# Performance work log

Measured on AMD Instinct MI355X. Metric: run time of the kernel, lower is better.

## Reference

```python
import jax, jax.numpy as jnp
import numpy as np

B, T, D, H = 64, 512, 256, 1024
INIT_S = 0.005


def setup_inputs() -> dict:
    key = jax.random.key(0)
    ks = jax.random.split(key, 8)
    gate_bias = float(np.log(INIT_S / (1.0 - INIT_S)))
    # Linear weights in torch layout [out, in]; y = x @ W.T + b.
    # Gate weights (Ws, Us) are zero-init in the module; we use small random
    # values so the gate path actually exercises the math.
    return {
        "x": jax.random.normal(ks[0], (B, T, D), dtype=jnp.float32),
        "Wx_w": jax.random.normal(ks[1], (H, D), dtype=jnp.float32) / np.sqrt(D),
        "Wx_b": jnp.zeros((H,), dtype=jnp.float32),
        "Wh_w": jax.random.normal(ks[2], (H, H), dtype=jnp.float32) / np.sqrt(H),
        "Ws_w": jax.random.normal(ks[3], (1, D), dtype=jnp.float32) * 0.01,
        "Ws_b": jnp.full((1,), gate_bias, dtype=jnp.float32),
        "Us_w": jax.random.normal(ks[4], (1, H), dtype=jnp.float32) * 0.01,
        "out_w": jax.random.normal(ks[5], (1, H), dtype=jnp.float32) / np.sqrt(H),
        "out_b": jnp.zeros((1,), dtype=jnp.float32),
    }


def reference(x, Wx_w, Wx_b, Wh_w, Ws_w, Ws_b, Us_w, out_w, out_b):
    # SharedGateRNN.forward_with_intermediates (ln=False, gate_rescale=None)
    wh_diag = jnp.diagonal(Wh_w)        # [H]
    us_vec = Us_w.reshape(-1)           # [H]

    def step(h_prev, x_t):
        # x_t: [B, D], h_prev: [B, H]
        a_s = x_t @ Ws_w.T + Ws_b + h_prev @ Us_w.T     # [B, 1]
        s = jax.nn.sigmoid(a_s)                          # [B, 1] scalar gate
        pre = x_t @ Wx_w.T + Wx_b + h_prev @ Wh_w.T      # [B, H]
        h_tilde = jnp.tanh(pre)
        h = (1.0 - s) * h_prev + s * h_tilde             # broadcast gate over H
        y = h @ out_w.T + out_b                          # [B, 1]
        gate_s = jnp.broadcast_to(s, h.shape)
        leak = 1.0 - gate_s
        tanh_prime = 1.0 - h_tilde ** 2
        s_prime = s * (1.0 - s)                          # [B, 1]
        rdiag = (h_tilde - h_prev) * (s_prime * us_vec) + s * tanh_prime * wh_diag
        return h, (y, h, gate_s, leak, rdiag)

    h0 = jnp.zeros((x.shape[0], H), dtype=x.dtype)
    x_t_first = jnp.transpose(x, (1, 0, 2))              # [T, B, D]
    _, (ys, hs, gates, leaks, rdiags) = jax.lax.scan(step, h0, x_t_first)

    swap = lambda a: jnp.transpose(a, (1, 0, 2))         # [T,B,*] -> [B,T,*]
    return (swap(ys), swap(hs), swap(gates), swap(leaks), swap(rdiags))
```

## Files before the change

### kernel.cpp

```cpp
#include <hip/hip_runtime.h>

#define NT 512
#define ND 256
#define NH 1024
#define NB 64

typedef float f32x4 __attribute__((ext_vector_type(4)));
typedef short bf16x8 __attribute__((ext_vector_type(8)));

__device__ __forceinline__ unsigned short f2bf(float f) {
  unsigned u = __builtin_bit_cast(unsigned, f);
  u += 0x7fffu + ((u >> 16) & 1u);
  return (unsigned short)(u >> 16);
}
__device__ __forceinline__ float bflo(unsigned u) {
  return __builtin_bit_cast(float, u << 16);
}
__device__ __forceinline__ float bfhi(unsigned u) {
  return __builtin_bit_cast(float, u & 0xffff0000u);
}
__device__ __forceinline__ bf16x8 pack8(float4 a, float4 b) {
  bf16x8 r;
  r[0] = (short)f2bf(a.x); r[1] = (short)f2bf(a.y);
  r[2] = (short)f2bf(a.z); r[3] = (short)f2bf(a.w);
  r[4] = (short)f2bf(b.x); r[5] = (short)f2bf(b.y);
  r[6] = (short)f2bf(b.z); r[7] = (short)f2bf(b.w);
  return r;
}

__global__ void __launch_bounds__(256, 1)
rnn_step_kernel(const float* __restrict__ x,
                const float* __restrict__ Wx_w,
                const float* __restrict__ Wx_b,
                const float* __restrict__ Wh_w,
                const float* __restrict__ Ws_w,
                const float* __restrict__ Ws_b,
                const float* __restrict__ Us_w,
                float* __restrict__ out,
                unsigned short* __restrict__ hbuf,
                unsigned int* __restrict__ flags)
{
  const int tid = (int)threadIdx.x;
  const int w   = tid >> 6;
  const int l   = tid & 63;
  const int bm  = l & 15;
  const int lg  = l >> 4;
  const int sl  = (int)blockIdx.x & 63;
  const int bg  = (int)blockIdx.x >> 6;
  const int r_base = sl * 16;
  const int b_base = bg * 16;
  const int ro = tid & 15;
  const int bo = tid >> 4;
  const int rg = r_base + ro;
  const int b_glob = b_base + bo;

  __shared__ unsigned short us_sh[1024];
  __shared__ float cpart[4][4][72];
  __shared__ float gpart[4][16];

  {
    const float4 uv = *(const float4*)(Us_w + tid*4);
    us_sh[tid*4+0] = f2bf(uv.x); us_sh[tid*4+1] = f2bf(uv.y);
    us_sh[tid*4+2] = f2bf(uv.z); us_sh[tid*4+3] = f2bf(uv.w);
  }

  bf16x8 whf[8];
  bf16x8 wxf[2];
  float4 wsf[4];
  {
    const int ar = r_base + bm;
    #pragma unroll
    for (int m = 0; m < 8; ++m) {
      const int k0 = w*256 + m*32 + lg*8;
      const float4 f0 = *(const float4*)(Wh_w + (size_t)ar*NH + k0);
      const float4 f1 = *(const float4*)(Wh_w + (size_t)ar*NH + k0 + 4);
      whf[m] = pack8(f0, f1);
    }
    #pragma unroll
    for (int m = 0; m < 2; ++m) {
      const int k0 = w*64 + m*32 + lg*8;
      const float4 f0 = *(const float4*)(Wx_w + (size_t)ar*ND + k0);
      const float4 f1 = *(const float4*)(Wx_w + (size_t)ar*ND + k0 + 4);
      wxf[m] = pack8(f0, f1);
      wsf[m*2]   = *(const float4*)(Ws_w + k0);
      wsf[m*2+1] = *(const float4*)(Ws_w + k0 + 4);
    }
  }
  const float wxb_r = Wx_b[rg];
  const float whd_r = Wh_w[(size_t)rg*NH + rg];
  const float usr_r = Us_w[rg];
  const float wsb   = Ws_b[0];

  float* const hs_o = out + (size_t)NB*NT;
  float* const g_o  = hs_o + (size_t)NB*NT*NH;
  float* const l_o  = g_o  + (size_t)NB*NT*NH;
  float* const rd_o = l_o  + (size_t)NB*NT*NH;

  __syncthreads();

  float myh = 0.f;
  float p_sg = 0.f, p_htld = 0.f, p_hp = 0.f;

  for (int t = 0; t < NT; ++t) {
    f32x4 acc = {0.f, 0.f, 0.f, 0.f};
    float ga = 0.f;
    {
      const float* xrow = x + ((size_t)(b_base+bm)*NT + t)*ND + w*64 + lg*8;
      #pragma unroll
      for (int m = 0; m < 2; ++m) {
        const float4 f0 = *(const float4*)(xrow + m*32);
        const float4 f1 = *(const float4*)(xrow + m*32 + 4);
        acc = __builtin_amdgcn_mfma_f32_16x16x32_bf16(
                wxf[m], pack8(f0, f1), acc, 0, 0, 0);
        ga += wsf[m*2].x*f0.x + wsf[m*2].y*f0.y + wsf[m*2].z*f0.z + wsf[m*2].w*f0.w
            + wsf[m*2+1].x*f1.x + wsf[m*2+1].y*f1.y + wsf[m*2+1].z*f1.z + wsf[m*2+1].w*f1.w;
      }
    }

    if (t > 0) {
      {
        const unsigned int* fp = flags + ((size_t)bg*NT + (t-1))*64 + l;
        while (true) {
          unsigned int v;
          asm volatile("global_load_dword %0, %1, off sc0 sc1\n\t"
                       "s_waitcnt vmcnt(0)"
                       : "=v"(v) : "v"(fp) : "memory");
          if (__all((int)(v != 0u))) break;
          __builtin_amdgcn_s_sleep(1);
        }
      }
      __builtin_amdgcn_sched_barrier(0);
      const unsigned short* hrow =
          hbuf + ((size_t)((t-1)&1)*NB + b_base + bm)*NH + w*256 + lg*8;
      uint4 hv[8];
      #pragma unroll
      for (int m = 0; m < 8; ++m)
        asm volatile("global_load_dwordx4 %0, %1, off sc0 sc1"
                     : "=v"(hv[m]) : "v"(hrow + m*32) : "memory");
      {
        const size_t obase = ((size_t)b_glob*NT + (t-1))*NH + rg;
        const float sp  = p_sg * (1.f - p_sg);
        const float rdv = (p_htld - p_hp)*(sp*usr_r) +
                          p_sg*(1.f - p_htld*p_htld)*whd_r;
        const float lv  = 1.f - p_sg;
        asm volatile("global_store_dword %0, %1, off nt"
                     :: "v"(hs_o + obase), "v"(myh) : "memory");
        asm volatile("global_store_dword %0, %1, off nt"
                     :: "v"(g_o + obase), "v"(p_sg) : "memory");
        asm volatile("global_store_dword %0, %1, off nt"
                     :: "v"(l_o + obase), "v"(lv) : "memory");
        asm volatile("global_store_dword %0, %1, off nt"
                     :: "v"(rd_o + obase), "v"(rdv) : "memory");
      }
      asm volatile("s_waitcnt vmcnt(4)" ::: "memory");
      __builtin_amdgcn_sched_barrier(0);
      #pragma unroll
      for (int m = 0; m < 8; ++m) {
        acc = __builtin_amdgcn_mfma_f32_16x16x32_bf16(
                whf[m], __builtin_bit_cast(bf16x8, hv[m]), acc, 0, 0, 0);
        const uint4 uu = *(const uint4*)&us_sh[w*256 + m*32 + lg*8];
        ga += bflo(uu.x)*bflo(hv[m].x) + bfhi(uu.x)*bfhi(hv[m].x)
            + bflo(uu.y)*bflo(hv[m].y) + bfhi(uu.y)*bfhi(hv[m].y)
            + bflo(uu.z)*bflo(hv[m].z) + bfhi(uu.z)*bfhi(hv[m].z)
            + bflo(uu.w)*bflo(hv[m].w) + bfhi(uu.w)*bfhi(hv[m].w);
      }
    }

    ga += __shfl_xor(ga, 16, 64);
    ga += __shfl_xor(ga, 32, 64);
    if (l < 16) gpart[w][l] = ga;
    cpart[w][0][l] = acc[0];
    cpart[w][1][l] = acc[1];
    cpart[w][2][l] = acc[2];
    cpart[w][3][l] = acc[3];
    __syncthreads();

    const float gsum = gpart[0][bo] + gpart[1][bo] + gpart[2][bo] + gpart[3][bo];
    const int ci = ro & 3, cl = ((ro >> 2) << 4) + bo;
    const float pre0 = cpart[0][ci][cl] + cpart[1][ci][cl] +
                       cpart[2][ci][cl] + cpart[3][ci][cl];
    const float sg   = 1.f / (1.f + expf(-(gsum + wsb)));
    const float pre  = pre0 + wxb_r;
    const float htld = tanhf(pre);
    const float hp   = myh;
    const float h    = (1.f - sg)*hp + sg*htld;
    myh = h; p_sg = sg; p_htld = htld; p_hp = hp;
    {
      const unsigned hb = (unsigned)f2bf(h);
      unsigned short* hptr = hbuf + ((size_t)(t & 1)*NB + b_glob)*NH + rg;
      asm volatile("global_store_short %0, %1, off sc0 sc1"
                   :: "v"(hptr), "v"(hb) : "memory");
    }
    asm volatile("s_waitcnt vmcnt(0)" ::: "memory");
    __syncthreads();
    if (tid == 0) {
      unsigned int one = 1u;
      unsigned int* fp = flags + ((size_t)bg*NT + t)*64 + sl;
      asm volatile("global_store_dword %0, %1, off sc0 sc1"
                   :: "v"(fp), "v"(one) : "memory");
    }
  }

  {
    const size_t obase = ((size_t)b_glob*NT + (NT-1))*NH + rg;
    const float sp  = p_sg * (1.f - p_sg);
    const float rdv = (p_htld - p_hp)*(sp*usr_r) +
                      p_sg*(1.f - p_htld*p_htld)*whd_r;
    __builtin_nontemporal_store(myh, &hs_o[obase]);
    __builtin_nontemporal_store(p_sg, &g_o[obase]);
    __builtin_nontemporal_store(1.f - p_sg, &l_o[obase]);
    __builtin_nontemporal_store(rdv, &rd_o[obase]);
  }
}

__global__ void yfinish_kernel(const float* __restrict__ hs,
                               const float* __restrict__ out_w,
                               const float* __restrict__ out_b,
                               float* __restrict__ ys)
{
  const int row  = (int)blockIdx.x*4 + ((int)threadIdx.x >> 6);
  const int lane = (int)threadIdx.x & 63;
  const float4* hp = (const float4*)(hs + (size_t)row*NH);
  const float4* wp = (const float4*)out_w;
  float s = 0.f;
  #pragma unroll
  for (int i = 0; i < 4; ++i) {
    const float4 h4 = hp[i*64 + lane];
    const float4 w4 = wp[i*64 + lane];
    s += h4.x*w4.x + h4.y*w4.y + h4.z*w4.z + h4.w*w4.w;
  }
  #pragma unroll
  for (int off = 32; off > 0; off >>= 1) s += __shfl_xor(s, off, 64);
  if (lane == 0) ys[row] = s + out_b[0];
}

extern "C" void kernel_launch(void* const* d_in, const int* in_sizes, int n_in,
                              void* d_out, int out_size, void* d_ws, size_t ws_size,
                              hipStream_t stream)
{
  (void)in_sizes; (void)n_in; (void)out_size; (void)ws_size;
  const float* x     = (const float*)d_in[0];
  const float* Wx_w  = (const float*)d_in[1];
  const float* Wx_b  = (const float*)d_in[2];
  const float* Wh_w  = (const float*)d_in[3];
  const float* Ws_w  = (const float*)d_in[4];
  const float* Ws_b  = (const float*)d_in[5];
  const float* Us_w  = (const float*)d_in[6];
  const float* out_w = (const float*)d_in[7];
  const float* out_b = (const float*)d_in[8];
  float* out = (float*)d_out;

  char* ws = (char*)d_ws;
  unsigned short* hbuf = (unsigned short*)ws;
  unsigned int* flags  = (unsigned int*)(ws + 262144);

  hipMemsetAsync(flags, 0, (size_t)4*NT*64*sizeof(unsigned int), stream);
  rnn_step_kernel<<<dim3(256), dim3(256), 0, stream>>>(
      x, Wx_w, Wx_b, Wh_w, Ws_w, Ws_b, Us_w, out, hbuf, flags);
  yfinish_kernel<<<dim3((NB*NT)/4), dim3(256), 0, stream>>>(
      out + (size_t)NB*NT, out_w, out_b, out);
}
```

Measured before the change: 1.819 ms.

## Repartition RNN step across 128 blocks of 512 threads with 32 rows each

```diff
diff --git a/kernel.cpp b/kernel.cpp
--- a/kernel.cpp
+++ b/kernel.cpp
@@ -28,7 +28,7 @@
   return r;
 }
 
-__global__ void __launch_bounds__(256, 1)
+__global__ void __launch_bounds__(512, 1)
 rnn_step_kernel(const float* __restrict__ x,
                 const float* __restrict__ Wx_w,
                 const float* __restrict__ Wx_b,
@@ -45,46 +45,47 @@
   const int l   = tid & 63;
   const int bm  = l & 15;
   const int lg  = l >> 4;
-  const int sl  = (int)blockIdx.x & 63;
-  const int bg  = (int)blockIdx.x >> 6;
-  const int r_base = sl * 16;
+  const int sl  = (int)blockIdx.x & 31;
+  const int bg  = (int)blockIdx.x >> 5;
+  const int r_base = sl * 32;
   const int b_base = bg * 16;
-  const int ro = tid & 15;
-  const int bo = tid >> 4;
+  const int ro = tid & 31;
+  const int bo = tid >> 5;
   const int rg = r_base + ro;
   const int b_glob = b_base + bo;
 
   __shared__ unsigned short us_sh[1024];
-  __shared__ float cpart[4][4][72];
-  __shared__ float gpart[4][16];
-
-  {
+  __shared__ float cpart[8][8][72];
+  __shared__ float gpart[8][16];
+
+  if (tid < 256) {
     const float4 uv = *(const float4*)(Us_w + tid*4);
     us_sh[tid*4+0] = f2bf(uv.x); us_sh[tid*4+1] = f2bf(uv.y);
     us_sh[tid*4+2] = f2bf(uv.z); us_sh[tid*4+3] = f2bf(uv.w);
   }
 
-  bf16x8 whf[8];
+  bf16x8 whf[2][4];
   bf16x8 wxf[2];
-  float4 wsf[4];
+  float4 wsf0, wsf1;
   {
-    const int ar = r_base + bm;
     #pragma unroll
-    for (int m = 0; m < 8; ++m) {
-      const int k0 = w*256 + m*32 + lg*8;
-      const float4 f0 = *(const float4*)(Wh_w + (size_t)ar*NH + k0);
-      const float4 f1 = *(const float4*)(Wh_w + (size_t)ar*NH + k0 + 4);
-      whf[m] = pack8(f0, f1);
-    }
-    #pragma unroll
-    for (int m = 0; m < 2; ++m) {
-      const int k0 = w*64 + m*32 + lg*8;
-      const float4 f0 = *(const float4*)(Wx_w + (size_t)ar*ND + k0);
-      const float4 f1 = *(const float4*)(Wx_w + (size_t)ar*ND + k0 + 4);
-      wxf[m] = pack8(f0, f1);
-      wsf[m*2]   = *(const float4*)(Ws_w + k0);
-      wsf[m*2+1] = *(const float4*)(Ws_w + k0 + 4);
-    }
+    for (int rb = 0; rb < 2; ++rb) {
+      const int ar = r_base + rb*16 + bm;
+      #pragma unroll
+      for (int m = 0; m < 4; ++m) {
+        const int k0 = w*128 + m*32 + lg*8;
+        const float4 f0 = *(const float4*)(Wh_w + (size_t)ar*NH + k0);
+        const float4 f1 = *(const float4*)(Wh_w + (size_t)ar*NH + k0 + 4);
+        whf[rb][m] = pack8(f0, f1);
+      }
+      const int kx = w*32 + lg*8;
+      const float4 g0 = *(const float4*)(Wx_w + (size_t)ar*ND + kx);
+      const float4 g1 = *(const float4*)(Wx_w + (size_t)ar*ND + kx + 4);
+      wxf[rb] = pack8(g0, g1);
+    }
+    const int kx = w*32 + lg*8;
+    wsf0 = *(const float4*)(Ws_w + kx);
+    wsf1 = *(const float4*)(Ws_w + kx + 4);
   }
   const float wxb_r = Wx_b[rg];
   const float whd_r = Wh_w[(size_t)rg*NH + rg];
@@ -102,24 +103,23 @@
   float p_sg = 0.f, p_htld = 0.f, p_hp = 0.f;
 
   for (int t = 0; t < NT; ++t) {
-    f32x4 acc = {0.f, 0.f, 0.f, 0.f};
+    f32x4 acc0 = {0.f, 0.f, 0.f, 0.f};
+    f32x4 acc1 = {0.f, 0.f, 0.f, 0.f};
     float ga = 0.f;
     {
-      const float* xrow = x + ((size_t)(b_base+bm)*NT + t)*ND + w*64 + lg*8;
-      #pragma unroll
-      for (int m = 0; m < 2; ++m) {
-        const float4 f0 = *(const float4*)(xrow + m*32);
-        const float4 f1 = *(const float4*)(xrow + m*32 + 4);
-        acc = __builtin_amdgcn_mfma_f32_16x16x32_bf16(
-                wxf[m], pack8(f0, f1), acc, 0, 0, 0);
-        ga += wsf[m*2].x*f0.x + wsf[m*2].y*f0.y + wsf[m*2].z*f0.z + wsf[m*2].w*f0.w
-            + wsf[m*2+1].x*f1.x + wsf[m*2+1].y*f1.y + wsf[m*2+1].z*f1.z + wsf[m*2+1].w*f1.w;
-      }
+      const float* xrow = x + ((size_t)(b_base+bm)*NT + t)*ND + w*32 + lg*8;
+      const float4 f0 = *(const float4*)(xrow);
+      const float4 f1 = *(const float4*)(xrow + 4);
+      const bf16x8 xb = pack8(f0, f1);
+      acc0 = __builtin_amdgcn_mfma_f32_16x16x32_bf16(wxf[0], xb, acc0, 0, 0, 0);
+      acc1 = __builtin_amdgcn_mfma_f32_16x16x32_bf16(wxf[1], xb, acc1, 0, 0, 0);
+      ga += wsf0.x*f0.x + wsf0.y*f0.y + wsf0.z*f0.z + wsf0.w*f0.w
+          + wsf1.x*f1.x + wsf1.y*f1.y + wsf1.z*f1.z + wsf1.w*f1.w;
     }
 
     if (t > 0) {
       {
-        const unsigned int* fp = flags + ((size_t)bg*NT + (t-1))*64 + l;
+        const unsigned int* fp = flags + ((size_t)bg*NT + (t-1))*32 + (l & 31);
         while (true) {
           unsigned int v;
           asm volatile("global_load_dword %0, %1, off sc0 sc1\n\t"
@@ -131,10 +131,10 @@
       }
       __builtin_amdgcn_sched_barrier(0);
       const unsigned short* hrow =
-          hbuf + ((size_t)((t-1)&1)*NB + b_base + bm)*NH + w*256 + lg*8;
-      uint4 hv[8];
-      #pragma unroll
-      for (int m = 0; m < 8; ++m)
+          hbuf + ((size_t)((t-1)&1)*NB + b_base + bm)*NH + w*128 + lg*8;
+      uint4 hv[4];
+      #pragma unroll
+      for (int m = 0; m < 4; ++m)
         asm volatile("global_load_dwordx4 %0, %1, off sc0 sc1"
                      : "=v"(hv[m]) : "v"(hrow + m*32) : "memory");
       {
@@ -155,10 +155,11 @@
       asm volatile("s_waitcnt vmcnt(4)" ::: "memory");
       __builtin_amdgcn_sched_barrier(0);
       #pragma unroll
-      for (int m = 0; m < 8; ++m) {
-        acc = __builtin_amdgcn_mfma_f32_16x16x32_bf16(
-                whf[m], __builtin_bit_cast(bf16x8, hv[m]), acc, 0, 0, 0);
-        const uint4 uu = *(const uint4*)&us_sh[w*256 + m*32 + lg*8];
+      for (int m = 0; m < 4; ++m) {
+        const bf16x8 hb = __builtin_bit_cast(bf16x8, hv[m]);
+        acc0 = __builtin_amdgcn_mfma_f32_16x16x32_bf16(whf[0][m], hb, acc0, 0, 0, 0);
+        acc1 = __builtin_amdgcn_mfma_f32_16x16x32_bf16(whf[1][m], hb, acc1, 0, 0, 0);
+        const uint4 uu = *(const uint4*)&us_sh[w*128 + m*32 + lg*8];
         ga += bflo(uu.x)*bflo(hv[m].x) + bfhi(uu.x)*bfhi(hv[m].x)
             + bflo(uu.y)*bflo(hv[m].y) + bfhi(uu.y)*bfhi(hv[m].y)
             + bflo(uu.z)*bflo(hv[m].z) + bfhi(uu.z)*bfhi(hv[m].z)
@@ -169,16 +170,24 @@
     ga += __shfl_xor(ga, 16, 64);
     ga += __shfl_xor(ga, 32, 64);
     if (l < 16) gpart[w][l] = ga;
-    cpart[w][0][l] = acc[0];
-    cpart[w][1][l] = acc[1];
-    cpart[w][2][l] = acc[2];
-    cpart[w][3][l] = acc[3];
+    #pragma unroll
+    for (int r = 0; r < 4; ++r) {
+      cpart[w][r][l]     = acc0[r];
+      cpart[w][4 + r][l] = acc1[r];
+    }
     __syncthreads();
 
-    const float gsum = gpart[0][bo] + gpart[1][bo] + gpart[2][bo] + gpart[3][bo];
-    const int ci = ro & 3, cl = ((ro >> 2) << 4) + bo;
-    const float pre0 = cpart[0][ci][cl] + cpart[1][ci][cl] +
-                       cpart[2][ci][cl] + cpart[3][ci][cl];
+    float gsum = 0.f, pre0 = 0.f;
+    {
+      const int rb = ro >> 4, rr = ro & 15;
+      const int slot = rb*4 + (rr & 3);
+      const int cl   = ((rr >> 2) << 4) | bo;
+      #pragma unroll
+      for (int ww = 0; ww < 8; ++ww) {
+        gsum += gpart[ww][bo];
+        pre0 += cpart[ww][slot][cl];
+      }
+    }
     const float sg   = 1.f / (1.f + expf(-(gsum + wsb)));
     const float pre  = pre0 + wxb_r;
     const float htld = tanhf(pre);
@@ -195,7 +204,7 @@
     __syncthreads();
     if (tid == 0) {
       unsigned int one = 1u;
-      unsigned int* fp = flags + ((size_t)bg*NT + t)*64 + sl;
+      unsigned int* fp = flags + ((size_t)bg*NT + t)*32 + sl;
       asm volatile("global_store_dword %0, %1, off sc0 sc1"
                    :: "v"(fp), "v"(one) : "memory");
     }
@@ -254,8 +263,8 @@
   unsigned short* hbuf = (unsigned short*)ws;
   unsigned int* flags  = (unsigned int*)(ws + 262144);
 
-  hipMemsetAsync(flags, 0, (size_t)4*NT*64*sizeof(unsigned int), stream);
-  rnn_step_kernel<<<dim3(256), dim3(256), 0, stream>>>(
+  hipMemsetAsync(flags, 0, (size_t)4*NT*32*sizeof(unsigned int), stream);
+  rnn_step_kernel<<<dim3(128), dim3(512), 0, stream>>>(
       x, Wx_w, Wx_b, Wh_w, Ws_w, Ws_b, Us_w, out, hbuf, flags);
   yfinish_kernel<<<dim3((NB*NT)/4), dim3(256), 0, stream>>>(
       out + (size_t)NB*NT, out_w, out_b, out);
```

Result: slower. 1.923 ms (+5.7%).

## Prefetch next-step x rows and issue early speculative flag load

Applied to the files above, without the earlier changes.

```diff
diff --git a/kernel.cpp b/kernel.cpp
--- a/kernel.cpp
+++ b/kernel.cpp
@@ -100,34 +100,44 @@
 
   float myh = 0.f;
   float p_sg = 0.f, p_htld = 0.f, p_hp = 0.f;
+  unsigned flagv = 0;
+  float4 xq0, xq1, xq2, xq3;
+
+  {
+    const float* xr = x + ((size_t)(b_base + bm)*NT + 0)*ND + w*64 + lg*8;
+    asm volatile(
+      "global_load_dwordx4 %0, %4, off\n\t"
+      "global_load_dwordx4 %1, %4, off offset:16\n\t"
+      "global_load_dwordx4 %2, %4, off offset:128\n\t"
+      "global_load_dwordx4 %3, %4, off offset:144\n\t"
+      "s_waitcnt vmcnt(0)"
+      : "=&v"(xq0), "=&v"(xq1), "=&v"(xq2), "=&v"(xq3)
+      : "v"(xr) : "memory");
+    __builtin_amdgcn_sched_barrier(0);
+  }
 
   for (int t = 0; t < NT; ++t) {
     f32x4 acc = {0.f, 0.f, 0.f, 0.f};
-    float ga = 0.f;
-    {
-      const float* xrow = x + ((size_t)(b_base+bm)*NT + t)*ND + w*64 + lg*8;
-      #pragma unroll
-      for (int m = 0; m < 2; ++m) {
-        const float4 f0 = *(const float4*)(xrow + m*32);
-        const float4 f1 = *(const float4*)(xrow + m*32 + 4);
-        acc = __builtin_amdgcn_mfma_f32_16x16x32_bf16(
-                wxf[m], pack8(f0, f1), acc, 0, 0, 0);
-        ga += wsf[m*2].x*f0.x + wsf[m*2].y*f0.y + wsf[m*2].z*f0.z + wsf[m*2].w*f0.w
-            + wsf[m*2+1].x*f1.x + wsf[m*2+1].y*f1.y + wsf[m*2+1].z*f1.z + wsf[m*2+1].w*f1.w;
-      }
-    }
+    float ga = wsf[0].x*xq0.x + wsf[0].y*xq0.y + wsf[0].z*xq0.z + wsf[0].w*xq0.w
+             + wsf[1].x*xq1.x + wsf[1].y*xq1.y + wsf[1].z*xq1.z + wsf[1].w*xq1.w
+             + wsf[2].x*xq2.x + wsf[2].y*xq2.y + wsf[2].z*xq2.z + wsf[2].w*xq2.w
+             + wsf[3].x*xq3.x + wsf[3].y*xq3.y + wsf[3].z*xq3.z + wsf[3].w*xq3.w;
+    acc = __builtin_amdgcn_mfma_f32_16x16x32_bf16(wxf[0], pack8(xq0, xq1), acc, 0, 0, 0);
+    acc = __builtin_amdgcn_mfma_f32_16x16x32_bf16(wxf[1], pack8(xq2, xq3), acc, 0, 0, 0);
+
+    const int tn = (t + 1 < NT) ? (t + 1) : t;
+    const float* xrn = x + ((size_t)(b_base + bm)*NT + tn)*ND + w*64 + lg*8;
 
     if (t > 0) {
-      {
+      asm volatile("s_waitcnt vmcnt(0)" ::: "memory");
+      if (!__all((int)(flagv != 0u))) {
         const unsigned int* fp = flags + ((size_t)bg*NT + (t-1))*64 + l;
-        while (true) {
-          unsigned int v;
+        do {
+          __builtin_amdgcn_s_sleep(1);
           asm volatile("global_load_dword %0, %1, off sc0 sc1\n\t"
                        "s_waitcnt vmcnt(0)"
-                       : "=v"(v) : "v"(fp) : "memory");
-          if (__all((int)(v != 0u))) break;
-          __builtin_amdgcn_s_sleep(1);
-        }
+                       : "=v"(flagv) : "v"(fp) : "memory");
+        } while (!__all((int)(flagv != 0u)));
       }
       __builtin_amdgcn_sched_barrier(0);
       const unsigned short* hrow =
@@ -152,7 +162,14 @@
         asm volatile("global_store_dword %0, %1, off nt"
                      :: "v"(rd_o + obase), "v"(rdv) : "memory");
       }
-      asm volatile("s_waitcnt vmcnt(4)" ::: "memory");
+      asm volatile(
+        "global_load_dwordx4 %0, %4, off\n\t"
+        "global_load_dwordx4 %1, %4, off offset:16\n\t"
+        "global_load_dwordx4 %2, %4, off offset:128\n\t"
+        "global_load_dwordx4 %3, %4, off offset:144"
+        : "=&v"(xq0), "=&v"(xq1), "=&v"(xq2), "=&v"(xq3)
+        : "v"(xrn) : "memory");
+      asm volatile("s_waitcnt vmcnt(8)" ::: "memory");
       __builtin_amdgcn_sched_barrier(0);
       #pragma unroll
       for (int m = 0; m < 8; ++m) {
@@ -164,6 +181,14 @@
             + bflo(uu.z)*bflo(hv[m].z) + bfhi(uu.z)*bfhi(hv[m].z)
             + bflo(uu.w)*bflo(hv[m].w) + bfhi(uu.w)*bfhi(hv[m].w);
       }
+    } else {
+      asm volatile(
+        "global_load_dwordx4 %0, %4, off\n\t"
+        "global_load_dwordx4 %1, %4, off offset:16\n\t"
+        "global_load_dwordx4 %2, %4, off offset:128\n\t"
+        "global_load_dwordx4 %3, %4, off offset:144"
+        : "=&v"(xq0), "=&v"(xq1), "=&v"(xq2), "=&v"(xq3)
+        : "v"(xrn) : "memory");
     }
 
     ga += __shfl_xor(ga, 16, 64);
@@ -192,12 +217,18 @@
                    :: "v"(hptr), "v"(hb) : "memory");
     }
     asm volatile("s_waitcnt vmcnt(0)" ::: "memory");
+    __builtin_amdgcn_sched_barrier(0);
     __syncthreads();
     if (tid == 0) {
       unsigned int one = 1u;
       unsigned int* fp = flags + ((size_t)bg*NT + t)*64 + sl;
       asm volatile("global_store_dword %0, %1, off sc0 sc1"
                    :: "v"(fp), "v"(one) : "memory");
+    }
+    {
+      const unsigned int* fld = flags + ((size_t)bg*NT + t)*64 + l;
+      asm volatile("global_load_dword %0, %1, off sc0 sc1"
+                   : "=v"(flagv) : "v"(fld) : "memory");
     }
   }
 
```

After: 3.240 ms. +78.2%, slower.
